# Performance work log

Hardware: AMD Instinct MI355X
Metric: run time of the kernel (lower is better)

The kernel has to match this reference:

```python
import jax, jax.numpy as jnp
import numpy as np
from jax import lax

H, W = 2048, 2048
KS = 3            # spatial NMS / centroid kernel size
EPS_NMS = 1e-5    # NMS3d eps (threshold=0 branch)
EPS_DIV = 1e-8
BORDER = 1        # int(mrSize=1.0)


def _grid_weights():
    # generate_3dgrid(3, 3, 3) centered: coords = linspace(-k/2+1, k/2, k) = [-0.5, 0.5, 1.5]
    c = np.linspace(-KS / 2 + 1, KS / 2, KS).astype(np.float32)
    g2 = np.stack([np.repeat(c, KS), np.tile(c, KS)], 1)                              # [9,2] (y,x), y-major
    g3 = np.concatenate([np.repeat(c, KS * KS)[:, None], np.tile(g2, (KS, 1))], 1)    # [27,3] (z,y,x)
    # grid.t().view(3,3,3,3): out-channel c holds coordinate c over the 3x3x3 cube (OIHW)
    return jnp.asarray(g3.T.reshape(3, 3, KS, KS))


def _border_mask():
    m = np.ones((H, W), np.float32)
    m[:BORDER] = 0; m[H - BORDER:] = 0; m[:, :BORDER] = 0; m[:, W - BORDER:] = 0
    return jnp.asarray(m)


def setup_inputs() -> dict:
    key = jax.random.key(0)
    k1, k2, k3, k4 = jax.random.split(key, 4)
    return {
        "low": jax.random.uniform(k1, (1, 1, H, W), jnp.float32),
        "cur": jax.random.uniform(k2, (1, 1, H, W), jnp.float32),
        "high": jax.random.uniform(k3, (1, 1, H, W), jnp.float32),
        "aff_resp": jax.random.normal(k4, (1, 4, H, W), jnp.float32),
        "octaveMap": jnp.zeros((1, 1, H, W), jnp.float32),
        "num_features": 4096,
    }


def _core(low, cur, high, aff_resp, octaveMap, num_features):
    resp3d = jnp.concatenate([low, cur, high], axis=1)  # [1,3,H,W] scale cube
    # MaxPool3d(kernel=3, stride=1, padding=(0,1,1)) over (scale,H,W) -> [1,1,H,W]
    mp = lax.reduce_window(resp3d, -jnp.inf, lax.max,
                           (1, 3, 3, 3), (1, 1, 1, 1),
                           [(0, 0), (0, 0), (1, 1), (1, 1)])
    nms = (resp3d - mp + EPS_NMS > 0).astype(resp3d.dtype) * resp3d  # broadcast over 3 scales
    # keep only the center scale, zero 1px border, mask already-taken octave positions
    nmsed = nms[:, 1:2] * _border_mask() * (1.0 - octaveMap)          # [1,1,H,W]
    vals, idxs = lax.top_k(nmsed.reshape(-1), num_features)          # fixed-k selection branch
    # centroid fit: coordinate-weighted 3x3x3 sums / mass via conv2d over the 3 scale channels
    gw = _grid_weights()
    num = lax.conv_general_dilated(resp3d, gw, (1, 1), [(1, 1), (1, 1)])
    den = lax.conv_general_dilated(resp3d, jnp.ones((3, 3, KS, KS), resp3d.dtype),
                                   (1, 1), [(1, 1), (1, 1)])
    sc = num / (den + EPS_DIV)  # [1,3,H,W] = (scale, dy, dx)
    yy, xx = jnp.meshgrid(jnp.arange(H, dtype=sc.dtype), jnp.arange(W, dtype=sc.dtype), indexing="ij")
    sc = jnp.stack([sc[0, 0], sc[0, 1] + yy, sc[0, 2] + xx], 0).reshape(3, -1).T  # [H*W,3]
    sc = sc[idxs] / jnp.array([float(min(H, W)), float(H), float(W)], sc.dtype)   # normalize (s,y,x)
    A = aff_resp.reshape(4, -1).T[idxs].reshape(-1, 2, 2)   # gather per-keypoint affine
    A = sc[:, 0][:, None, None] * A                          # scale * A
    center_xy = jnp.stack([sc[:, 2], sc[:, 1]], axis=1)[:, :, None]  # (x, y) column
    lafs = jnp.concatenate([A, center_xy], axis=2)           # [K,2,3] LAFs
    return vals, lafs, nmsed


def reference(low, cur, high, aff_resp, octaveMap, num_features):
    vals, lafs, nmsed = _core(low, cur, high, aff_resp, octaveMap, num_features)
    octave_new = (octaveMap + nmsed).astype(jnp.uint8)  # updated octave occupancy map
    return vals, lafs, octave_new
```

## Files before the change

### kernel.cpp

```cpp
#include <hip/hip_runtime.h>
#include <cstdint>
#include <cstddef>

#define HH 2048
#define WW 2048
#define NPIX (HH * WW)
#define EPS_NMS 1e-5f
#define EPS_DIV 1e-8f
#define NEG_INF (-3.402823466e+38f)
#define ROWS 8
#define LCAP 2048
#define SG_CAP 8192
#define NBIN 2048
#define SEL_BLOCKS 64
#define RB_ELEMS 32

typedef unsigned long long u64;


__device__ __forceinline__ float max3(float a, float b, float c) {
    return fmaxf(a, fmaxf(b, c));
}

__device__ __forceinline__ unsigned int aload(const unsigned int* p) {
    return __hip_atomic_load(p, __ATOMIC_RELAXED, __HIP_MEMORY_SCOPE_AGENT);
}

__device__ __forceinline__ void gbar(unsigned int* ctr) {
    __syncthreads();
    if (threadIdx.x == 0) {
        __threadfence();
        atomicAdd(ctr, 1u);
        while (aload(ctr) < (unsigned int)SEL_BLOCKS) {}
        __threadfence();
    }
    __syncthreads();
}

__global__ __launch_bounds__(256) void nms_map_kernel(
    const float* __restrict__ low, const float* __restrict__ cur,
    const float* __restrict__ high, const float* __restrict__ oct,
    float* __restrict__ oct_out, float* __restrict__ vals_out, int n7k,
    u64* __restrict__ cand, unsigned int* __restrict__ cnt, unsigned int cap)
{
    __shared__ unsigned int lcount, lbase;
    __shared__ u64 lcand[LCAP];

    const int tid = threadIdx.x;
    const int lane = tid & 63;
    const int x4 = blockIdx.x * 1024 + tid * 4;
    const int y0 = blockIdx.y * ROWS;
    if (tid == 0) lcount = 0u;

    if (blockIdx.y == 0) {
        int n4 = n7k >> 2;
        float4* vz = (float4*)vals_out;
        for (int i = blockIdx.x * 256 + tid; i < n4; i += gridDim.x * 256)
            vz[i] = make_float4(0.f, 0.f, 0.f, 0.f);
    }
    __syncthreads();

    float4 Lb[2], Cb[2], Hb[2], Ob[2];
    float eLl[2], eLc[2], eLh[2], eRl[2], eRc[2], eRh[2];

    #define ISSUE(t, slot) {                                                      \
        int tt = (t);                                                             \
        if (tt >= 0 && tt < HH) {                                                 \
            int jj = tt * WW + x4;                                                \
            Lb[slot] = *(const float4*)(low  + jj);                               \
            Cb[slot] = *(const float4*)(cur  + jj);                               \
            Hb[slot] = *(const float4*)(high + jj);                               \
            bool doL = (lane == 0)  && (x4 > 0);                                  \
            bool doR = (lane == 63) && (x4 + 4 < WW);                             \
            eLl[slot] = doL ? low[jj - 1]  : NEG_INF;                             \
            eLc[slot] = doL ? cur[jj - 1]  : NEG_INF;                             \
            eLh[slot] = doL ? high[jj - 1] : NEG_INF;                             \
            eRl[slot] = doR ? low[jj + 4]  : NEG_INF;                             \
            eRc[slot] = doR ? cur[jj + 4]  : NEG_INF;                             \
            eRh[slot] = doR ? high[jj + 4] : NEG_INF;                             \
        } else {                                                                  \
            Lb[slot] = Cb[slot] = Hb[slot] =                                      \
                make_float4(NEG_INF, NEG_INF, NEG_INF, NEG_INF);                  \
            eLl[slot] = eLc[slot] = eLh[slot] = NEG_INF;                          \
            eRl[slot] = eRc[slot] = eRh[slot] = NEG_INF;                          \
        }                                                                         \
    }

    #define CONSUME(slot, hzO, cvO) {                                             \
        float4 l = Lb[slot], c = Cb[slot], hh = Hb[slot];                         \
        float4 z;                                                                 \
        z.x = max3(l.x, c.x, hh.x);                                               \
        z.y = max3(l.y, c.y, hh.y);                                               \
        z.z = max3(l.z, c.z, hh.z);                                               \
        z.w = max3(l.w, c.w, hh.w);                                               \
        float zeL = max3(eLl[slot], eLc[slot], eLh[slot]);                        \
        float zeR = max3(eRl[slot], eRc[slot], eRh[slot]);                        \
        float zl = __shfl_up(z.w, 1, 64);                                         \
        float zr = __shfl_down(z.x, 1, 64);                                       \
        if (lane == 0)  zl = zeL;                                                 \
        if (lane == 63) zr = zeR;                                                 \
        hzO.x = max3(zl,  z.x, z.y);                                              \
        hzO.y = max3(z.x, z.y, z.z);                                              \
        hzO.z = max3(z.y, z.z, z.w);                                              \
        hzO.w = max3(z.z, z.w, zr);                                               \
        cvO = c;                                                                  \
    }

    float4 hzA, hzB, hzC, cvB, cvC, cvT;
    ISSUE(y0 - 1, 0)
    ISSUE(y0,     1)
    Ob[0] = *(const float4*)(oct + y0 * WW + x4);
    CONSUME(0, hzA, cvT)
    ISSUE(y0 + 1, 0)
    CONSUME(1, hzB, cvB)

    #pragma unroll
    for (int j = 0; j < ROWS; ++j) {
        int y = y0 + j;
        ISSUE(y + 2, (j + 1) & 1)
        if (j + 1 < ROWS)
            Ob[(j + 1) & 1] = *(const float4*)(oct + (y + 1) * WW + x4);
        CONSUME(j & 1, hzC, cvC)

        int idx = y * WW + x4;
        float4 o = Ob[j & 1];
        bool yin = (y > 0) && (y < HH - 1);
        float4 ov;
        #define DO_COMP(comp, i)  {                                               \
            float m = max3(hzA.comp, hzB.comp, hzC.comp);                         \
            int xg = x4 + (i);                                                    \
            bool interior = yin && (xg > 0) && (xg < WW - 1);                     \
            float nm = (((cvB.comp - m + EPS_NMS) > 0.0f) && interior)            \
                       ? cvB.comp * (1.0f - o.comp) : 0.0f;                       \
            ov.comp = (float)((unsigned char)(o.comp + nm));                      \
            if (nm > 0.0f) {                                                      \
                unsigned int p = atomicAdd(&lcount, 1u);                          \
                if (p < LCAP)                                                     \
                    lcand[p] = (((u64)__float_as_uint(nm)) << 32)                 \
                               | (unsigned int)(~(idx + (i)));                    \
            }                                                                     \
        }
        DO_COMP(x, 0) DO_COMP(y, 1) DO_COMP(z, 2) DO_COMP(w, 3)
        #undef DO_COMP
        *(float4*)(oct_out + idx) = ov;
        hzA = hzB; hzB = hzC; cvB = cvC;
    }
    #undef ISSUE
    #undef CONSUME

    __syncthreads();
    unsigned int c = lcount < LCAP ? lcount : LCAP;
    if (tid == 0) lbase = atomicAdd(cnt, c);
    __syncthreads();
    unsigned int base = lbase;
    for (unsigned int i = tid; i < c; i += 256) {
        unsigned int p = base + i;
        if (p < cap) cand[p] = lcand[i];
    }
}

__global__ __launch_bounds__(256) void select_kernel(
    const u64* __restrict__ cand, u64* __restrict__ SG,
    unsigned int* __restrict__ cnt, unsigned int* __restrict__ hist,
    unsigned int cap, int K)
{
    __shared__ unsigned int h[NBIN];
    __shared__ unsigned int s[256];
    __shared__ unsigned int sh_prefix, sh_remk;
    __shared__ unsigned int lc, lb;
    __shared__ u64 buf[2048];
    const int tid = threadIdx.x;
    const int bid = blockIdx.x;
    unsigned int* bar = cnt + 16;
    unsigned int n = cnt[0]; if (n > cap) n = cap;
    const unsigned int stride = SEL_BLOCKS * 256;

    int gtid = bid * 256 + tid;
    if (gtid < NBIN) hist[gtid] = 0u;
    for (int i = tid; i < NBIN; i += 256) h[i] = 0u;
    __syncthreads();

    for (unsigned int i = bid * 256 + tid; i < n; i += stride)
        atomicAdd(&h[(unsigned int)(cand[i] >> 53)], 1u);
    gbar(&bar[0]);
    for (int i = tid; i < NBIN; i += 256) { unsigned int v = h[i]; if (v) atomicAdd(&hist[i], v); }
    gbar(&bar[1]);

    if (bid == 0) {
        unsigned int bins[8], csum = 0;
        #pragma unroll
        for (int i = 0; i < 8; ++i) { bins[i] = aload(&hist[tid * 8 + i]); csum += bins[i]; }
        s[tid] = csum;
        __syncthreads();
        for (int off = 1; off < 256; off <<= 1) {
            unsigned int v = (tid + off < 256) ? s[tid + off] : 0u;
            __syncthreads(); s[tid] += v; __syncthreads();
        }
        unsigned int remk = (unsigned int)K;
        unsigned int incl = s[tid], excl = incl - csum, total = s[0];
        if (incl >= remk && excl < remk) {
            unsigned int cum = excl; int b = 7;
            for (; b > 0; --b) { cum += bins[b]; if (cum >= remk) break; }
            if (cum < remk) cum += bins[0];
            sh_prefix = (unsigned int)(tid * 8 + b);
            sh_remk   = remk - (cum - bins[b]);
        }
        if (tid == 0 && total < remk) { sh_prefix = 0u; sh_remk = remk; }
        __syncthreads();
        for (int i = tid; i < NBIN; i += 256) hist[i] = 0u;
        __syncthreads();
        if (tid == 0) atomicExch(&cnt[3], sh_prefix);
    }
    gbar(&bar[2]);

    unsigned int prefix = aload(&cnt[3]);
    for (int i = tid; i < NBIN; i += 256) h[i] = 0u;
    __syncthreads();
    for (unsigned int i = bid * 256 + tid; i < n; i += stride) {
        unsigned int k32 = (unsigned int)(cand[i] >> 32);
        if ((k32 >> 21) == prefix) atomicAdd(&h[(k32 >> 10) & (NBIN - 1u)], 1u);
    }
    __syncthreads();
    for (int i = tid; i < NBIN; i += 256) { unsigned int v = h[i]; if (v) atomicAdd(&hist[i], v); }
    gbar(&bar[3]);

    if (bid == 0) {
        unsigned int bins[8], csum = 0;
        #pragma unroll
        for (int i = 0; i < 8; ++i) { bins[i] = aload(&hist[tid * 8 + i]); csum += bins[i]; }
        s[tid] = csum;
        __syncthreads();
        for (int off = 1; off < 256; off <<= 1) {
            unsigned int v = (tid + off < 256) ? s[tid + off] : 0u;
            __syncthreads(); s[tid] += v; __syncthreads();
        }
        unsigned int remk = sh_remk, pfx = sh_prefix;
        unsigned int incl = s[tid], excl = incl - csum, total = s[0];
        __shared__ unsigned int sh_T;
        if (tid == 0) sh_T = pfx << 11;
        __syncthreads();
        if (incl >= remk && excl < remk) {
            unsigned int cum = excl; int b = 7;
            for (; b > 0; --b) { cum += bins[b]; if (cum >= remk) break; }
            if (cum < remk) cum += bins[0];
            sh_T = (pfx << 11) | (unsigned int)(tid * 8 + b);
        }
        __syncthreads();
        if (tid == 0) atomicExch(&cnt[3], sh_T);
    }
    gbar(&bar[4]);

    unsigned int T = aload(&cnt[3]);
    if (tid == 0) lc = 0u;
    __syncthreads();
    for (unsigned int i = bid * 256 + tid; i < n; i += stride) {
        u64 key = cand[i];
        if ((unsigned int)(key >> 42) >= T) {
            unsigned int p = atomicAdd(&lc, 1u);
            if (p < 2048u) buf[p] = key;
        }
    }
    __syncthreads();
    unsigned int c = lc < 2048u ? lc : 2048u;
    if (tid == 0) lb = atomicAdd(&cnt[1], c);
    __syncthreads();
    unsigned int base = lb;
    for (unsigned int i = tid; i < c; i += 256) {
        unsigned int p = base + i;
        if (p < SG_CAP) SG[p] = buf[i];
    }
}

__global__ __launch_bounds__(256) void rank_finalize_kernel(
    const u64* __restrict__ SG, const unsigned int* __restrict__ cnt,
    const float* __restrict__ low, const float* __restrict__ cur,
    const float* __restrict__ high, const float* __restrict__ aff,
    float* __restrict__ out, int K)
{
    __shared__ u64 s[SG_CAP];
    __shared__ unsigned int rnk[RB_ELEMS];
    unsigned int m = cnt[1]; if (m > SG_CAP) m = SG_CAP;
    unsigned int base = blockIdx.x * RB_ELEMS;
    if (base >= m) return;
    for (unsigned int i = threadIdx.x; i < m; i += 256) s[i] = SG[i];
    __syncthreads();

    unsigned int wave = threadIdx.x >> 6, lane = threadIdx.x & 63u;
    u64 my[8];
    unsigned int r[8];
    #pragma unroll
    for (int i = 0; i < 8; ++i) {
        unsigned int e = base + wave * 8 + i;
        my[i] = (e < m) ? s[e] : ~0ull;
        r[i] = 0u;
    }
    for (unsigned int j = lane; j < m; j += 64) {
        u64 key = s[j];
        #pragma unroll
        for (int i = 0; i < 8; ++i) r[i] += (unsigned)(key > my[i]);
    }
    #pragma unroll
    for (int i = 0; i < 8; ++i) {
        #pragma unroll
        for (int off = 32; off > 0; off >>= 1)
            r[i] += __shfl_down(r[i], off, 64);
        if (lane == 0) rnk[wave * 8 + i] = r[i];
    }
    __syncthreads();

    int i = threadIdx.x;
    if (i >= RB_ELEMS) return;
    unsigned int e = base + (unsigned int)i;
    if (e >= m) return;
    unsigned int rank = rnk[i];
    if (rank >= (unsigned int)K) return;
    u64 my_key = s[e];

    float val = __uint_as_float((unsigned int)(my_key >> 32));
    unsigned int idx = ~((unsigned int)my_key);
    out[rank] = val;
    float* laf = out + K + (size_t)rank * 6;
    int y = (int)(idx >> 11), x = (int)(idx & (WW - 1));
    const float ccw[3] = {-0.5f, 0.5f, 1.5f};
    float den = 0.0f, nz = 0.0f, ny = 0.0f, nx = 0.0f;
    #pragma unroll
    for (int dy = -1; dy <= 1; ++dy) {
        int yy = y + dy;
        if (yy < 0 || yy >= HH) continue;
        #pragma unroll
        for (int dx = -1; dx <= 1; ++dx) {
            int xx = x + dx;
            if (xx < 0 || xx >= WW) continue;
            int jj = yy * WW + xx;
            float v0 = low[jj], v1 = cur[jj], v2 = high[jj];
            float ssum = v0 + v1 + v2;
            den += ssum;
            nz += -0.5f * v0 + 0.5f * v1 + 1.5f * v2;
            ny += ccw[dy + 1] * ssum;
            nx += ccw[dx + 1] * ssum;
        }
    }
    float inv = 1.0f / (den + EPS_DIV);
    float s_n = (nz * inv) * (1.0f / 2048.0f);
    float y_n = (ny * inv + (float)y) * (1.0f / 2048.0f);
    float x_n = (nx * inv + (float)x) * (1.0f / 2048.0f);
    float a0 = aff[idx], a1 = aff[NPIX + idx], a2 = aff[2 * NPIX + idx], a3 = aff[3 * NPIX + idx];
    laf[0] = s_n * a0; laf[1] = s_n * a1; laf[2] = x_n;
    laf[3] = s_n * a2; laf[4] = s_n * a3; laf[5] = y_n;
}

extern "C" void kernel_launch(void* const* d_in, const int* in_sizes, int n_in,
                              void* d_out, int out_size, void* d_ws, size_t ws_size,
                              hipStream_t stream) {
    const float* low  = (const float*)d_in[0];
    const float* cur  = (const float*)d_in[1];
    const float* high = (const float*)d_in[2];
    const float* aff  = (const float*)d_in[3];
    const float* oct  = (const float*)d_in[4];
    int K = (out_size - NPIX) / 7;
    float* out = (float*)d_out;

    char* ws = (char*)d_ws;
    unsigned int* cnt  = (unsigned int*)ws;
    unsigned int* hist = (unsigned int*)(ws + 128);
    u64* SG            = (u64*)(ws + 16384);
    const size_t cand_off = 81920;
    u64* cand          = (u64*)(ws + cand_off);
    size_t cap_sz = ws_size > cand_off ? (ws_size - cand_off) / 8 : 0;
    if (cap_sz > (size_t)NPIX) cap_sz = (size_t)NPIX;
    unsigned int cap = (unsigned int)cap_sz;

    hipMemsetAsync(ws, 0, 128, stream);

    dim3 gb(WW / 1024, HH / ROWS, 1);
    nms_map_kernel<<<gb, 256, 0, stream>>>(low, cur, high, oct, out + (size_t)7 * K,
                                           out, 7 * K, cand, cnt, cap);
    select_kernel<<<SEL_BLOCKS, 256, 0, stream>>>(cand, SG, cnt, hist, cap, K);
    rank_finalize_kernel<<<SG_CAP / RB_ELEMS, 256, 0, stream>>>(SG, cnt, low, cur, high, aff, out, K);
}
```

Measured before the change: 202.0 us.

## Fuse select and rank-finalize kernels and shrink NMS row tiles

Merges the select and rank/finalize kernels into one persistent kernel that uses a grid barrier, saving a launch and reusing shared memory (histogram and buffer aliased into the sorted-candidate array). Select blocks grow from 64 to 256, and the SG cap shrinks to 7936 so that 256 blocks of 32 ranks cover it. The NMS kernel processes 2 rows per block instead of 8, giving four times as many blocks and skipping the redundant last-row prefetch. Fewer rows per block means more halo reloads, and a grid barrier across 256 blocks only works if every block is resident at once.

```diff
diff --git a/kernel.cpp b/kernel.cpp
--- a/kernel.cpp
+++ b/kernel.cpp
@@ -8,11 +8,11 @@
 #define EPS_NMS 1e-5f
 #define EPS_DIV 1e-8f
 #define NEG_INF (-3.402823466e+38f)
-#define ROWS 8
-#define LCAP 2048
-#define SG_CAP 8192
+#define ROWS 2
+#define LCAP 512
+#define SG_CAP 7936
 #define NBIN 2048
-#define SEL_BLOCKS 64
+#define SEL_BLOCKS 256
 #define RB_ELEMS 32
 
 typedef unsigned long long u64;
@@ -117,9 +117,10 @@
     #pragma unroll
     for (int j = 0; j < ROWS; ++j) {
         int y = y0 + j;
-        ISSUE(y + 2, (j + 1) & 1)
-        if (j + 1 < ROWS)
+        if (j + 1 < ROWS) {
+            ISSUE(y + 2, (j + 1) & 1)
             Ob[(j + 1) & 1] = *(const float4*)(oct + (y + 1) * WW + x4);
+        }
         CONSUME(j & 1, hzC, cvC)
 
         int idx = y * WW + x4;
@@ -159,16 +160,21 @@
     }
 }
 
-__global__ __launch_bounds__(256) void select_kernel(
+__global__ __launch_bounds__(256) void select_rank_kernel(
     const u64* __restrict__ cand, u64* __restrict__ SG,
     unsigned int* __restrict__ cnt, unsigned int* __restrict__ hist,
-    unsigned int cap, int K)
+    unsigned int cap, int K,
+    const float* __restrict__ low, const float* __restrict__ cur,
+    const float* __restrict__ high, const float* __restrict__ aff,
+    float* __restrict__ out)
 {
-    __shared__ unsigned int h[NBIN];
+    __shared__ u64 sgl[SG_CAP];
     __shared__ unsigned int s[256];
-    __shared__ unsigned int sh_prefix, sh_remk;
-    __shared__ unsigned int lc, lb;
-    __shared__ u64 buf[2048];
+    __shared__ unsigned int rnk[RB_ELEMS];
+    __shared__ unsigned int sh_prefix, sh_remk, lc, lb;
+    unsigned int* h = (unsigned int*)sgl;
+    u64* buf = sgl + 2048;
+
     const int tid = threadIdx.x;
     const int bid = blockIdx.x;
     unsigned int* bar = cnt + 16;
@@ -269,33 +275,25 @@
         unsigned int p = base + i;
         if (p < SG_CAP) SG[p] = buf[i];
     }
-}
-
-__global__ __launch_bounds__(256) void rank_finalize_kernel(
-    const u64* __restrict__ SG, const unsigned int* __restrict__ cnt,
-    const float* __restrict__ low, const float* __restrict__ cur,
-    const float* __restrict__ high, const float* __restrict__ aff,
-    float* __restrict__ out, int K)
-{
-    __shared__ u64 s[SG_CAP];
-    __shared__ unsigned int rnk[RB_ELEMS];
-    unsigned int m = cnt[1]; if (m > SG_CAP) m = SG_CAP;
-    unsigned int base = blockIdx.x * RB_ELEMS;
-    if (base >= m) return;
-    for (unsigned int i = threadIdx.x; i < m; i += 256) s[i] = SG[i];
-    __syncthreads();
-
-    unsigned int wave = threadIdx.x >> 6, lane = threadIdx.x & 63u;
+    gbar(&bar[5]);
+
+    unsigned int m = aload(&cnt[1]); if (m > SG_CAP) m = SG_CAP;
+    unsigned int rbase = (unsigned int)bid * RB_ELEMS;
+    if (rbase >= m) return;
+    for (unsigned int i = tid; i < m; i += 256) sgl[i] = SG[i];
+    __syncthreads();
+
+    unsigned int wave = (unsigned int)tid >> 6, lane = (unsigned int)tid & 63u;
     u64 my[8];
     unsigned int r[8];
     #pragma unroll
     for (int i = 0; i < 8; ++i) {
-        unsigned int e = base + wave * 8 + i;
-        my[i] = (e < m) ? s[e] : ~0ull;
+        unsigned int e = rbase + wave * 8 + i;
+        my[i] = (e < m) ? sgl[e] : ~0ull;
         r[i] = 0u;
     }
     for (unsigned int j = lane; j < m; j += 64) {
-        u64 key = s[j];
+        u64 key = sgl[j];
         #pragma unroll
         for (int i = 0; i < 8; ++i) r[i] += (unsigned)(key > my[i]);
     }
@@ -308,13 +306,13 @@
     }
     __syncthreads();
 
-    int i = threadIdx.x;
+    int i = tid;
     if (i >= RB_ELEMS) return;
-    unsigned int e = base + (unsigned int)i;
+    unsigned int e = rbase + (unsigned int)i;
     if (e >= m) return;
     unsigned int rank = rnk[i];
     if (rank >= (unsigned int)K) return;
-    u64 my_key = s[e];
+    u64 my_key = sgl[e];
 
     float val = __uint_as_float((unsigned int)(my_key >> 32));
     unsigned int idx = ~((unsigned int)my_key);
@@ -375,6 +373,6 @@
     dim3 gb(WW / 1024, HH / ROWS, 1);
     nms_map_kernel<<<gb, 256, 0, stream>>>(low, cur, high, oct, out + (size_t)7 * K,
                                            out, 7 * K, cand, cnt, cap);
-    select_kernel<<<SEL_BLOCKS, 256, 0, stream>>>(cand, SG, cnt, hist, cap, K);
-    rank_finalize_kernel<<<SG_CAP / RB_ELEMS, 256, 0, stream>>>(SG, cnt, low, cur, high, aff, out, K);
-}
+    select_rank_kernel<<<SEL_BLOCKS, 256, 0, stream>>>(cand, SG, cnt, hist, cap, K,
+                                                       low, cur, high, aff, out);
+}
```

After: 282.3 us. +39.7%, slower.
